# Kernel tuning notes

Measured on AMD Instinct MI355X. Metric: run time of the kernel, lower is better.

Reference implementation:

```python
import jax, jax.numpy as jnp
import numpy as np

H = 32        # num_attention_heads
KVH = 8       # num_key_value_heads
D = 64        # attention_head_size
WIN = 256     # attention_window_size (left/right)
ROPE_BASE = 10000.0


def setup_inputs() -> dict:
    key = jax.random.key(0)
    k1, k2, k3 = jax.random.split(key, 3)
    B, S = 2, 2048
    return {
        "query_states": jax.random.normal(k1, (B, S, H * D), dtype=jnp.float32),
        "key_states": jax.random.normal(k2, (B, S, KVH * D), dtype=jnp.float32),
        "value_states": jax.random.normal(k3, (B, S, KVH * D), dtype=jnp.float32),
    }


def _rope_cos_sin(seq_len, dtype):
    inv_freq = 1.0 / (ROPE_BASE ** (jnp.arange(0, D, 2, dtype=jnp.float32) / D))  # [D/2]
    pos = jnp.arange(seq_len, dtype=jnp.float32)
    freqs = pos[:, None] * inv_freq[None, :]          # [S, D/2]
    emb = jnp.concatenate([freqs, freqs], axis=-1)    # [S, D]
    return jnp.cos(emb).astype(dtype), jnp.sin(emb).astype(dtype)


def _rotate_half(x):
    x1, x2 = x[..., : D // 2], x[..., D // 2 :]
    return jnp.concatenate([-x2, x1], axis=-1)


def reference(query_states, key_states, value_states):
    B, S, _ = query_states.shape
    n_rep = H // KVH

    q = query_states.reshape(B, S, H, D).transpose(0, 2, 1, 3)        # [B,H,S,D]
    k = key_states.reshape(B, S, KVH, D).transpose(0, 2, 1, 3)        # [B,KVH,S,D]
    v = value_states.reshape(B, S, KVH, D).transpose(0, 2, 1, 3)

    # repeat_kv: [B,KVH,S,D] -> [B,H,S,D]
    k = jnp.repeat(k, n_rep, axis=1)
    v = jnp.repeat(v, n_rep, axis=1)

    cos, sin = _rope_cos_sin(S, q.dtype)   # [S,D]
    cos = cos[None, None]                  # [1,1,S,D]
    sin = sin[None, None]
    q = q * cos + _rotate_half(q) * sin
    k = k * cos + _rotate_half(k) * sin

    scale = 1.0 / jnp.sqrt(jnp.asarray(D, dtype=q.dtype))
    scores = jnp.einsum("bhqd,bhkd->bhqk", q, k) * scale              # [B,H,S,S]

    i = jnp.arange(S)[:, None]
    j = jnp.arange(S)[None, :]
    allowed = (j >= i - WIN) & (j <= i)                               # [S,S]
    scores = jnp.where(allowed[None, None], scores, jnp.finfo(scores.dtype).min)

    probs = jax.nn.softmax(scores, axis=-1)
    out = jnp.einsum("bhqk,bhkd->bhqd", probs, v)                     # [B,H,S,D]
    return out.transpose(0, 2, 1, 3).reshape(B, S, H * D)
```

## Files before the change

kernel.cpp:

```cpp
#include <hip/hip_runtime.h>
#include <math.h>

#define NH   32
#define NKVH 8
#define HD   64
#define WIN  256
#define BB   2
#define SS   2048

typedef short short8 __attribute__((ext_vector_type(8)));
typedef float f32x4  __attribute__((ext_vector_type(4)));

__device__ __forceinline__ ushort f2bf(float x) {
    union { float f; unsigned u; } v; v.f = x;
    unsigned u = v.u + 0x7FFF + ((v.u >> 16) & 1);
    return (ushort)(u >> 16);
}

__global__ __launch_bounds__(256) void prep_kv(const float* __restrict__ K,
                                               const float* __restrict__ V,
                                               ushort* __restrict__ Kr,
                                               ushort* __restrict__ Vt) {
    __shared__ ushort tile[64][65];
    int bidx = blockIdx.x;
    int s0  = (bidx & 31) * 64;
    int kvh = (bidx >> 5) & 7;
    int b   = bidx >> 8;
    int d   = threadIdx.x & 63, g = threadIdx.x >> 6;

    float inv = __powf(10000.f, -(float)(d & 31) * (1.f / 32.f));
#pragma unroll
    for (int i = 0; i < 16; ++i) {
        int s = s0 + g * 16 + i;
        float kv = K[(size_t)(b * SS + s) * (NKVH * HD) + kvh * HD + d];
        float partner = __shfl(kv, d ^ 32, 64);
        float sn, cs;
        __sincosf((float)s * inv, &sn, &cs);
        float krot = kv * cs + ((d < 32) ? -partner : partner) * sn;
        Kr[((size_t)(b * NKVH + kvh) * SS + s) * HD + d] = f2bf(krot);
    }
#pragma unroll
    for (int i = 0; i < 16; ++i) {
        int sl = g * 16 + i;
        tile[sl][d] = f2bf(V[(size_t)(b * SS + s0 + sl) * (NKVH * HD) + kvh * HD + d]);
    }
    __syncthreads();
#pragma unroll
    for (int i = 0; i < 16; ++i) {
        int dr = g * 16 + i;
        Vt[((size_t)(b * NKVH + kvh) * HD + dr) * SS + s0 + d] = tile[d][dr];
    }
}

__global__ __launch_bounds__(256, 4) void attn_mfma(const float* __restrict__ Q,
                                                    const ushort* __restrict__ Kr,
                                                    const ushort* __restrict__ Vt,
                                                    float* __restrict__ O) {
    __shared__ ushort Pl[4][2][2][16][40];
    const int wv = threadIdx.x >> 6, lane = threadIdx.x & 63;
    const int lo16 = lane & 15, quad = lane >> 4;
    const int bidx = blockIdx.x;
    const int qblk = bidx & 63;
    const int kvh  = (bidx >> 6) & 7;
    const int b    = bidx >> 9;
    const int h    = kvh * 4 + wv;
    const int q0   = qblk * 32;

    float invf[8];
#pragma unroll
    for (int j = 0; j < 8; ++j)
        invf[j] = __powf(10000.f, -(float)(quad * 8 + j) * (1.f / 32.f));

    short8 aq[2][2];
#pragma unroll
    for (int t = 0; t < 2; ++t) {
        int qi = q0 + t * 16 + lo16;
        const float* qrow = Q + (size_t)(b * SS + qi) * (NH * HD) + h * HD;
        float lo[8], hi[8];
        *(float4*)(lo)     = *(const float4*)(qrow + quad * 8);
        *(float4*)(lo + 4) = *(const float4*)(qrow + quad * 8 + 4);
        *(float4*)(hi)     = *(const float4*)(qrow + 32 + quad * 8);
        *(float4*)(hi + 4) = *(const float4*)(qrow + 32 + quad * 8 + 4);
#pragma unroll
        for (int j = 0; j < 8; ++j) {
            float sn, cs;
            __sincosf((float)qi * invf[j], &sn, &cs);
            aq[t][0][j] = (short)f2bf((lo[j] * cs - hi[j] * sn) * 0.125f);
            aq[t][1][j] = (short)f2bf((hi[j] * cs + lo[j] * sn) * 0.125f);
        }
    }

    const ushort* kbase = Kr + (size_t)(b * NKVH + kvh) * SS * HD;
    const ushort* vbase = Vt + (size_t)(b * NKVH + kvh) * HD * SS;

    f32x4 acc[2][4];
#pragma unroll
    for (int t = 0; t < 2; ++t)
#pragma unroll
        for (int i = 0; i < 4; ++i) acc[t][i] = (f32x4){0.f, 0.f, 0.f, 0.f};
    float psum[2] = {0.f, 0.f};

    int klo = q0 - WIN; if (klo < 0) klo = 0;
    const int khi = q0 + 31;

    short8 kcur[4], knxt[4];
    {
        int key0 = klo + lo16, key1 = klo + 16 + lo16;
        kcur[0] = *(const short8*)(kbase + (size_t)key0 * HD + quad * 8);
        kcur[1] = *(const short8*)(kbase + (size_t)key0 * HD + 32 + quad * 8);
        kcur[2] = *(const short8*)(kbase + (size_t)key1 * HD + quad * 8);
        kcur[3] = *(const short8*)(kbase + (size_t)key1 * HD + 32 + quad * 8);
    }

    int buf = 0;
    for (int kb = klo; kb <= khi; kb += 32, buf ^= 1) {
        const f32x4 z = {0.f, 0.f, 0.f, 0.f};
        f32x4 s00 = __builtin_amdgcn_mfma_f32_16x16x32_bf16(kcur[0], aq[0][0], z,   0, 0, 0);
        s00       = __builtin_amdgcn_mfma_f32_16x16x32_bf16(kcur[1], aq[0][1], s00, 0, 0, 0);
        f32x4 s01 = __builtin_amdgcn_mfma_f32_16x16x32_bf16(kcur[2], aq[0][0], z,   0, 0, 0);
        s01       = __builtin_amdgcn_mfma_f32_16x16x32_bf16(kcur[3], aq[0][1], s01, 0, 0, 0);
        f32x4 s10 = __builtin_amdgcn_mfma_f32_16x16x32_bf16(kcur[0], aq[1][0], z,   0, 0, 0);
        s10       = __builtin_amdgcn_mfma_f32_16x16x32_bf16(kcur[1], aq[1][1], s10, 0, 0, 0);
        f32x4 s11 = __builtin_amdgcn_mfma_f32_16x16x32_bf16(kcur[2], aq[1][0], z,   0, 0, 0);
        s11       = __builtin_amdgcn_mfma_f32_16x16x32_bf16(kcur[3], aq[1][1], s11, 0, 0, 0);

#pragma unroll
        for (int t = 0; t < 2; ++t) {
            const f32x4 sa = t ? s10 : s00;
            const f32x4 sb = t ? s11 : s01;
            const int qtmin = q0 + t * 16;
            const int myq   = qtmin + lo16;
            float p[8];
            if ((kb + 31 > qtmin) || (kb < qtmin + 15 - WIN)) {
#pragma unroll
                for (int r = 0; r < 4; ++r) {
                    int key0 = kb + quad * 4 + r;
                    int key1 = key0 + 16;
                    p[r]     = (key0 <= myq && key0 >= myq - WIN) ? __expf(sa[r]) : 0.f;
                    p[4 + r] = (key1 <= myq && key1 >= myq - WIN) ? __expf(sb[r]) : 0.f;
                }
            } else {
#pragma unroll
                for (int r = 0; r < 4; ++r) { p[r] = __expf(sa[r]); p[4 + r] = __expf(sb[r]); }
            }
            psum[t] += ((p[0] + p[1]) + (p[2] + p[3])) + ((p[4] + p[5]) + (p[6] + p[7]));
            ushort4 u0 = make_ushort4(f2bf(p[0]), f2bf(p[1]), f2bf(p[2]), f2bf(p[3]));
            ushort4 u1 = make_ushort4(f2bf(p[4]), f2bf(p[5]), f2bf(p[6]), f2bf(p[7]));
            *(ushort4*)&Pl[wv][buf][t][lo16][quad * 4]      = u0;
            *(ushort4*)&Pl[wv][buf][t][lo16][16 + quad * 4] = u1;
        }

        {
            int key0 = kb + 32 + lo16; if (key0 > SS - 1) key0 = SS - 1;
            int key1 = key0 + 16;      if (key1 > SS - 1) key1 = SS - 1;
            knxt[0] = *(const short8*)(kbase + (size_t)key0 * HD + quad * 8);
            knxt[1] = *(const short8*)(kbase + (size_t)key0 * HD + 32 + quad * 8);
            knxt[2] = *(const short8*)(kbase + (size_t)key1 * HD + quad * 8);
            knxt[3] = *(const short8*)(kbase + (size_t)key1 * HD + 32 + quad * 8);
        }
        short8 vf[4];
        {
            int sb2 = kb + quad * 8; if (sb2 > SS - 8) sb2 = SS - 8;
#pragma unroll
            for (int i = 0; i < 4; ++i)
                vf[i] = *(const short8*)(vbase + (size_t)(i * 16 + lo16) * SS + sb2);
        }

        __asm__ volatile("s_waitcnt lgkmcnt(0)" ::: "memory");
        short8 ap0 = *(const short8*)&Pl[wv][buf][0][lo16][quad * 8];
        short8 ap1 = *(const short8*)&Pl[wv][buf][1][lo16][quad * 8];

#pragma unroll
        for (int i = 0; i < 4; ++i)
            acc[0][i] = __builtin_amdgcn_mfma_f32_16x16x32_bf16(ap0, vf[i], acc[0][i], 0, 0, 0);
#pragma unroll
        for (int i = 0; i < 4; ++i)
            acc[1][i] = __builtin_amdgcn_mfma_f32_16x16x32_bf16(ap1, vf[i], acc[1][i], 0, 0, 0);

#pragma unroll
        for (int i = 0; i < 4; ++i) kcur[i] = knxt[i];
    }

#pragma unroll
    for (int t = 0; t < 2; ++t) {
        float ps = psum[t];
        ps += __shfl_xor(ps, 16, 64);
        ps += __shfl_xor(ps, 32, 64);
#pragma unroll
        for (int r = 0; r < 4; ++r) {
            float invr = 1.f / __shfl(ps, quad * 4 + r, 16);
            int qr = q0 + t * 16 + quad * 4 + r;
            size_t orow = ((size_t)(b * SS + qr) * NH + h) * HD;
            O[orow + 0 * 16 + lo16] = acc[t][0][r] * invr;
            O[orow + 1 * 16 + lo16] = acc[t][1][r] * invr;
            O[orow + 2 * 16 + lo16] = acc[t][2][r] * invr;
            O[orow + 3 * 16 + lo16] = acc[t][3][r] * invr;
        }
    }
}

__device__ __forceinline__ float wave_sum(float x) {
#pragma unroll
    for (int off = 32; off > 0; off >>= 1) x += __shfl_xor(x, off, 64);
    return x;
}

__global__ __launch_bounds__(256) void attn_scalar(const float* __restrict__ Q,
                                                   const float* __restrict__ K,
                                                   const float* __restrict__ V,
                                                   float* __restrict__ O) {
    int wave = blockIdx.x * 4 + (threadIdx.x >> 6);
    int lane = threadIdx.x & 63;
    int q  = wave % SS;
    int bh = wave / SS;
    int h  = bh % NH;
    int b  = bh / NH;
    int kvh = h >> 2;

    float inv = __powf(10000.f, -(float)(lane & 31) * (1.f / 32.f));
    float sn, cs;
    __sincosf((float)q * inv, &sn, &cs);

    float qv = Q[(size_t)(b * SS + q) * (NH * HD) + h * HD + lane];
    float qpart = __shfl(qv, lane ^ 32, 64);
    float qrot = (qv * cs + ((lane < 32) ? -qpart : qpart) * sn) * 0.125f;

    const float* vbase = V + (size_t)b * SS * (NKVH * HD) + kvh * HD;
    float m = -1e30f, l = 0.f, acc = 0.f;
    int k0 = q - WIN; if (k0 < 0) k0 = 0;
    for (int k = k0; k <= q; ++k) {
        float kraw = K[(size_t)(b * SS + k) * (NKVH * HD) + kvh * HD + lane];
        float kpart = __shfl(kraw, lane ^ 32, 64);
        float ksn, kcs;
        __sincosf((float)k * inv, &ksn, &kcs);
        float kv = kraw * kcs + ((lane < 32) ? -kpart : kpart) * ksn;
        float vv = vbase[(size_t)k * (NKVH * HD) + lane];
        float score = wave_sum(qrot * kv);
        float mnew  = fmaxf(m, score);
        float alpha = __expf(m - mnew);
        float p     = __expf(score - mnew);
        l   = l * alpha + p;
        acc = acc * alpha + p * vv;
        m   = mnew;
    }
    O[(((size_t)(b * SS + q) * NH) + h) * HD + lane] = acc / l;
}

extern "C" void kernel_launch(void* const* d_in, const int* in_sizes, int n_in,
                              void* d_out, int out_size, void* d_ws, size_t ws_size,
                              hipStream_t stream) {
    const float* Q = (const float*)d_in[0];
    const float* K = (const float*)d_in[1];
    const float* V = (const float*)d_in[2];
    float* O = (float*)d_out;

    size_t kv_elems = (size_t)BB * NKVH * SS * HD;
    size_t need = 2 * kv_elems * sizeof(ushort);

    if (ws_size >= need) {
        ushort* Kr = (ushort*)d_ws;
        ushort* Vt = Kr + kv_elems;
        prep_kv<<<BB * NKVH * (SS / 64), 256, 0, stream>>>(K, V, Kr, Vt);
        attn_mfma<<<BB * NKVH * (SS / 32), 256, 0, stream>>>(Q, Kr, Vt, O);
    } else {
        attn_scalar<<<(BB * NH * SS) / 4, 256, 0, stream>>>(Q, K, V, O);
    }
}
```

Measured before the change: 133.7 us.

## Split key range across wave pairs and shrink prep_kv tiles

The attention kernel now gives each head to two waves that process alternating 32-key blocks, then combines their partial accumulators and row sums through shared memory before normalising. This doubles the grid and halves the serial loop length per wave, aiming for more parallelism and shorter latency chains, at the cost of an extra block-wide barrier and LDS reduction. The K/V prep kernel uses 32-row tiles with pairwise rotation loads and vectorised transposed stores, and the rope frequency is computed with expf instead of powf.

```diff
diff --git a/kernel.cpp b/kernel.cpp
--- a/kernel.cpp
+++ b/kernel.cpp
@@ -11,6 +11,8 @@
 typedef short short8 __attribute__((ext_vector_type(8)));
 typedef float f32x4  __attribute__((ext_vector_type(4)));
 
+#define NEG_LN_1E4_32 (-0.28782313662425572f)
+
 __device__ __forceinline__ ushort f2bf(float x) {
     union { float f; unsigned u; } v; v.f = x;
     unsigned u = v.u + 0x7FFF + ((v.u >> 16) & 1);
@@ -21,34 +23,47 @@
                                                const float* __restrict__ V,
                                                ushort* __restrict__ Kr,
                                                ushort* __restrict__ Vt) {
-    __shared__ ushort tile[64][65];
-    int bidx = blockIdx.x;
-    int s0  = (bidx & 31) * 64;
-    int kvh = (bidx >> 5) & 7;
-    int b   = bidx >> 8;
-    int d   = threadIdx.x & 63, g = threadIdx.x >> 6;
-
-    float inv = __powf(10000.f, -(float)(d & 31) * (1.f / 32.f));
-#pragma unroll
-    for (int i = 0; i < 16; ++i) {
-        int s = s0 + g * 16 + i;
-        float kv = K[(size_t)(b * SS + s) * (NKVH * HD) + kvh * HD + d];
-        float partner = __shfl(kv, d ^ 32, 64);
-        float sn, cs;
-        __sincosf((float)s * inv, &sn, &cs);
-        float krot = kv * cs + ((d < 32) ? -partner : partner) * sn;
-        Kr[((size_t)(b * NKVH + kvh) * SS + s) * HD + d] = f2bf(krot);
-    }
-#pragma unroll
-    for (int i = 0; i < 16; ++i) {
-        int sl = g * 16 + i;
-        tile[sl][d] = f2bf(V[(size_t)(b * SS + s0 + sl) * (NKVH * HD) + kvh * HD + d]);
+    __shared__ ushort tile[32][66];
+    const int bidx = blockIdx.x;
+    const int s0  = (bidx & 63) * 32;
+    const int kvh = (bidx >> 6) & 7;
+    const int b   = bidx >> 9;
+    const int t   = threadIdx.x;
+
+    {
+        int d = t & 31, r = t >> 5;
+        float inv = __expf((float)d * NEG_LN_1E4_32);
+#pragma unroll
+        for (int i = 0; i < 4; ++i) {
+            int s = s0 + r + 8 * i;
+            const float* krow = K + (size_t)(b * SS + s) * (NKVH * HD) + kvh * HD;
+            float x1 = krow[d], x2 = krow[d + 32];
+            float sn, cs;
+            __sincosf((float)s * inv, &sn, &cs);
+            ushort* kout = Kr + ((size_t)(b * NKVH + kvh) * SS + s) * HD;
+            kout[d]      = f2bf(x1 * cs - x2 * sn);
+            kout[d + 32] = f2bf(x2 * cs + x1 * sn);
+        }
+    }
+
+    {
+        int dv = t & 63, rv = t >> 6;
+#pragma unroll
+        for (int i = 0; i < 8; ++i) {
+            int sl = rv + 4 * i;
+            tile[sl][dv] = f2bf(V[(size_t)(b * SS + s0 + sl) * (NKVH * HD) + kvh * HD + dv]);
+        }
     }
     __syncthreads();
-#pragma unroll
-    for (int i = 0; i < 16; ++i) {
-        int dr = g * 16 + i;
-        Vt[((size_t)(b * NKVH + kvh) * HD + dr) * SS + s0 + d] = tile[d][dr];
+    {
+        int g = t & 7, dr0 = t >> 3;
+#pragma unroll
+        for (int half = 0; half < 2; ++half) {
+            int dr = dr0 + 32 * half;
+            ushort4 u = make_ushort4(tile[4 * g + 0][dr], tile[4 * g + 1][dr],
+                                     tile[4 * g + 2][dr], tile[4 * g + 3][dr]);
+            *(ushort4*)(Vt + ((size_t)(b * NKVH + kvh) * HD + dr) * SS + s0 + 4 * g) = u;
+        }
     }
 }
 
@@ -56,20 +71,20 @@
                                                     const ushort* __restrict__ Kr,
                                                     const ushort* __restrict__ Vt,
                                                     float* __restrict__ O) {
-    __shared__ ushort Pl[4][2][2][16][40];
+    __shared__ ushort Pl[4][2][16][40];
+    __shared__ float  Cb[2][64][36];
+
     const int wv = threadIdx.x >> 6, lane = threadIdx.x & 63;
     const int lo16 = lane & 15, quad = lane >> 4;
+    const int ks   = wv & 1;
+    const int pair = wv >> 1;
     const int bidx = blockIdx.x;
-    const int qblk = bidx & 63;
-    const int kvh  = (bidx >> 6) & 7;
-    const int b    = bidx >> 9;
-    const int h    = kvh * 4 + wv;
-    const int q0   = qblk * 32;
-
-    float invf[8];
-#pragma unroll
-    for (int j = 0; j < 8; ++j)
-        invf[j] = __powf(10000.f, -(float)(quad * 8 + j) * (1.f / 32.f));
+    const int qblk  = bidx & 63;
+    const int hpair = (bidx >> 6) & 1;
+    const int kvh   = (bidx >> 7) & 7;
+    const int b     = bidx >> 10;
+    const int h     = kvh * 4 + hpair * 2 + pair;
+    const int q0    = qblk * 32;
 
     short8 aq[2][2];
 #pragma unroll
@@ -83,8 +98,9 @@
         *(float4*)(hi + 4) = *(const float4*)(qrow + 32 + quad * 8 + 4);
 #pragma unroll
         for (int j = 0; j < 8; ++j) {
+            float invf = __expf((float)(quad * 8 + j) * NEG_LN_1E4_32);
             float sn, cs;
-            __sincosf((float)qi * invf[j], &sn, &cs);
+            __sincosf((float)qi * invf, &sn, &cs);
             aq[t][0][j] = (short)f2bf((lo[j] * cs - hi[j] * sn) * 0.125f);
             aq[t][1][j] = (short)f2bf((hi[j] * cs + lo[j] * sn) * 0.125f);
         }
@@ -102,18 +118,18 @@
 
     int klo = q0 - WIN; if (klo < 0) klo = 0;
     const int khi = q0 + 31;
+    const int kb0 = klo + 32 * ks;
 
     short8 kcur[4], knxt[4];
     {
-        int key0 = klo + lo16, key1 = klo + 16 + lo16;
+        int key0 = kb0 + lo16, key1 = key0 + 16;
         kcur[0] = *(const short8*)(kbase + (size_t)key0 * HD + quad * 8);
         kcur[1] = *(const short8*)(kbase + (size_t)key0 * HD + 32 + quad * 8);
         kcur[2] = *(const short8*)(kbase + (size_t)key1 * HD + quad * 8);
         kcur[3] = *(const short8*)(kbase + (size_t)key1 * HD + 32 + quad * 8);
     }
 
-    int buf = 0;
-    for (int kb = klo; kb <= khi; kb += 32, buf ^= 1) {
+    for (int kb = kb0; kb <= khi; kb += 64) {
         const f32x4 z = {0.f, 0.f, 0.f, 0.f};
         f32x4 s00 = __builtin_amdgcn_mfma_f32_16x16x32_bf16(kcur[0], aq[0][0], z,   0, 0, 0);
         s00       = __builtin_amdgcn_mfma_f32_16x16x32_bf16(kcur[1], aq[0][1], s00, 0, 0, 0);
@@ -124,6 +140,22 @@
         f32x4 s11 = __builtin_amdgcn_mfma_f32_16x16x32_bf16(kcur[2], aq[1][0], z,   0, 0, 0);
         s11       = __builtin_amdgcn_mfma_f32_16x16x32_bf16(kcur[3], aq[1][1], s11, 0, 0, 0);
 
+        {
+            int key0 = kb + 64 + lo16; if (key0 > SS - 1) key0 = SS - 1;
+            int key1 = key0 + 16;      if (key1 > SS - 1) key1 = SS - 1;
+            knxt[0] = *(const short8*)(kbase + (size_t)key0 * HD + quad * 8);
+            knxt[1] = *(const short8*)(kbase + (size_t)key0 * HD + 32 + quad * 8);
+            knxt[2] = *(const short8*)(kbase + (size_t)key1 * HD + quad * 8);
+            knxt[3] = *(const short8*)(kbase + (size_t)key1 * HD + 32 + quad * 8);
+        }
+        short8 vf[4];
+        {
+            int sb2 = kb + quad * 8;
+#pragma unroll
+            for (int i = 0; i < 4; ++i)
+                vf[i] = *(const short8*)(vbase + (size_t)(i * 16 + lo16) * SS + sb2);
+        }
+
 #pragma unroll
         for (int t = 0; t < 2; ++t) {
             const f32x4 sa = t ? s10 : s00;
@@ -146,29 +178,13 @@
             psum[t] += ((p[0] + p[1]) + (p[2] + p[3])) + ((p[4] + p[5]) + (p[6] + p[7]));
             ushort4 u0 = make_ushort4(f2bf(p[0]), f2bf(p[1]), f2bf(p[2]), f2bf(p[3]));
             ushort4 u1 = make_ushort4(f2bf(p[4]), f2bf(p[5]), f2bf(p[6]), f2bf(p[7]));
-            *(ushort4*)&Pl[wv][buf][t][lo16][quad * 4]      = u0;
-            *(ushort4*)&Pl[wv][buf][t][lo16][16 + quad * 4] = u1;
-        }
-
-        {
-            int key0 = kb + 32 + lo16; if (key0 > SS - 1) key0 = SS - 1;
-            int key1 = key0 + 16;      if (key1 > SS - 1) key1 = SS - 1;
-            knxt[0] = *(const short8*)(kbase + (size_t)key0 * HD + quad * 8);
-            knxt[1] = *(const short8*)(kbase + (size_t)key0 * HD + 32 + quad * 8);
-            knxt[2] = *(const short8*)(kbase + (size_t)key1 * HD + quad * 8);
-            knxt[3] = *(const short8*)(kbase + (size_t)key1 * HD + 32 + quad * 8);
-        }
-        short8 vf[4];
-        {
-            int sb2 = kb + quad * 8; if (sb2 > SS - 8) sb2 = SS - 8;
-#pragma unroll
-            for (int i = 0; i < 4; ++i)
-                vf[i] = *(const short8*)(vbase + (size_t)(i * 16 + lo16) * SS + sb2);
+            *(ushort4*)&Pl[wv][t][lo16][quad * 4]      = u0;
+            *(ushort4*)&Pl[wv][t][lo16][16 + quad * 4] = u1;
         }
 
         __asm__ volatile("s_waitcnt lgkmcnt(0)" ::: "memory");
-        short8 ap0 = *(const short8*)&Pl[wv][buf][0][lo16][quad * 8];
-        short8 ap1 = *(const short8*)&Pl[wv][buf][1][lo16][quad * 8];
+        short8 ap0 = *(const short8*)&Pl[wv][0][lo16][quad * 8];
+        short8 ap1 = *(const short8*)&Pl[wv][1][lo16][quad * 8];
 
 #pragma unroll
         for (int i = 0; i < 4; ++i)
@@ -181,20 +197,46 @@
         for (int i = 0; i < 4; ++i) kcur[i] = knxt[i];
     }
 
+    float ps[2];
 #pragma unroll
     for (int t = 0; t < 2; ++t) {
-        float ps = psum[t];
-        ps += __shfl_xor(ps, 16, 64);
-        ps += __shfl_xor(ps, 32, 64);
-#pragma unroll
-        for (int r = 0; r < 4; ++r) {
-            float invr = 1.f / __shfl(ps, quad * 4 + r, 16);
-            int qr = q0 + t * 16 + quad * 4 + r;
-            size_t orow = ((size_t)(b * SS + qr) * NH + h) * HD;
-            O[orow + 0 * 16 + lo16] = acc[t][0][r] * invr;
-            O[orow + 1 * 16 + lo16] = acc[t][1][r] * invr;
-            O[orow + 2 * 16 + lo16] = acc[t][2][r] * invr;
-            O[orow + 3 * 16 + lo16] = acc[t][3][r] * invr;
+        float v = psum[t];
+        v += __shfl_xor(v, 16, 64);
+        v += __shfl_xor(v, 32, 64);
+        ps[t] = v;
+    }
+
+    if (ks == 1) {
+        float* cb = &Cb[pair][lane][0];
+#pragma unroll
+        for (int t = 0; t < 2; ++t)
+#pragma unroll
+            for (int i = 0; i < 4; ++i)
+                *(f32x4*)(cb + (t * 4 + i) * 4) = acc[t][i];
+        cb[32] = ps[0]; cb[33] = ps[1];
+    }
+    __syncthreads();
+    if (ks == 0) {
+        const float* cb = &Cb[pair][lane][0];
+#pragma unroll
+        for (int t = 0; t < 2; ++t)
+#pragma unroll
+            for (int i = 0; i < 4; ++i)
+                acc[t][i] += *(const f32x4*)(cb + (t * 4 + i) * 4);
+        ps[0] += cb[32]; ps[1] += cb[33];
+
+#pragma unroll
+        for (int t = 0; t < 2; ++t) {
+#pragma unroll
+            for (int r = 0; r < 4; ++r) {
+                float invr = 1.f / __shfl(ps[t], quad * 4 + r, 16);
+                int qr = q0 + t * 16 + quad * 4 + r;
+                size_t orow = ((size_t)(b * SS + qr) * NH + h) * HD;
+                O[orow + 0 * 16 + lo16] = acc[t][0][r] * invr;
+                O[orow + 1 * 16 + lo16] = acc[t][1][r] * invr;
+                O[orow + 2 * 16 + lo16] = acc[t][2][r] * invr;
+                O[orow + 3 * 16 + lo16] = acc[t][3][r] * invr;
+            }
         }
     }
 }
@@ -217,7 +259,7 @@
     int b  = bh / NH;
     int kvh = h >> 2;
 
-    float inv = __powf(10000.f, -(float)(lane & 31) * (1.f / 32.f));
+    float inv = __expf((float)(lane & 31) * NEG_LN_1E4_32);
     float sn, cs;
     __sincosf((float)q * inv, &sn, &cs);
 
@@ -260,8 +302,8 @@
     if (ws_size >= need) {
         ushort* Kr = (ushort*)d_ws;
         ushort* Vt = Kr + kv_elems;
-        prep_kv<<<BB * NKVH * (SS / 64), 256, 0, stream>>>(K, V, Kr, Vt);
-        attn_mfma<<<BB * NKVH * (SS / 32), 256, 0, stream>>>(Q, Kr, Vt, O);
+        prep_kv<<<BB * NKVH * (SS / 32), 256, 0, stream>>>(K, V, Kr, Vt);
+        attn_mfma<<<BB * NKVH * 2 * (SS / 32), 256, 0, stream>>>(Q, Kr, Vt, O);
     } else {
         attn_scalar<<<(BB * NH * SS) / 4, 256, 0, stream>>>(Q, K, V, O);
     }
```

Measured after the change: 143.6 us. +7.4%, slower.
